# Kernel optimization log

Hardware: AMD Instinct MI355X
Metric: run time of the kernel (lower is better)

The kernel has to match this reference:

```python
import jax, jax.numpy as jnp
import numpy as np

NUM_HEADS = 16
NEG = -10000000.0


def setup_inputs() -> dict:
    key = jax.random.key(0)
    k1, k2, k3 = jax.random.split(key, 3)
    B, N, C = 4, 2048, 1024
    inputs = jax.random.normal(k1, (B, N, C), dtype=jnp.float32)
    # learned params (xavier-ish scale)
    W_qkv = jax.random.normal(k2, (C, 3 * C), dtype=jnp.float32) * 0.02
    W_proj = jax.random.normal(k3, (C, C), dtype=jnp.float32) * 0.02
    b_proj = jnp.zeros((C,), dtype=jnp.float32)
    attn_mask = jnp.ones((N, N), dtype=jnp.int32)      # >0 means keep
    padding_mask = jnp.zeros((B, N), dtype=jnp.int32)  # >0 means mask out
    return {"inputs": inputs, "attn_mask": attn_mask, "padding_mask": padding_mask,
            "W_qkv": W_qkv, "W_proj": W_proj, "b_proj": b_proj}


def reference(inputs, attn_mask, padding_mask, W_qkv, W_proj, b_proj):
    B, N, C = inputs.shape
    H = NUM_HEADS
    d = C // H
    scale = d ** -0.5
    qkv = inputs @ W_qkv                                   # [B,N,3C]
    qkv = qkv.reshape(B, N, 3, H, d).transpose(2, 0, 3, 1, 4)  # [3,B,H,N,d]
    q, k, v = qkv[0], qkv[1], qkv[2]
    scores = jnp.einsum('bhqd,bhkd->bhqk', q, k) * scale   # [B,H,N,N]
    scores = jnp.where(attn_mask > 0, scores, NEG)
    pm = padding_mask[:, None, None, :]                    # [B,1,1,N]
    scores = jnp.where(pm > 0, NEG, scores)
    attn = jax.nn.softmax(scores, axis=-1)
    x = jnp.einsum('bhqk,bhkd->bhqd', attn, v)             # [B,H,N,d]
    x = x.swapaxes(1, 2).reshape(B, N, C)
    return x @ W_proj + b_proj
```

## Files before the change

kernel.cpp:

```cpp
#include <hip/hip_runtime.h>

#define NEG -10000000.0f
#define QSCALE 0.18033688011112042f

typedef __attribute__((ext_vector_type(8))) short bf16x8;
typedef __attribute__((ext_vector_type(4))) float f32x4;

static __device__ __forceinline__ short f2bf(float f) {
    unsigned int u = __float_as_uint(f);
    unsigned int r = (u + 0x7fffu + ((u >> 16) & 1u)) >> 16;
    return (short)r;
}

static __device__ __forceinline__ unsigned pack_bf16_2(float a, float b) {
    unsigned ua = __float_as_uint(a) + 0x8000u;
    unsigned ub = __float_as_uint(b) + 0x8000u;
    return __builtin_amdgcn_perm(ub, ua, 0x07060302u);
}

static __device__ __forceinline__ void async_cp16(const void* g, void* l) {
    __builtin_amdgcn_global_load_lds(
        (const __attribute__((address_space(1))) unsigned int*)g,
        (__attribute__((address_space(3))) unsigned int*)l, 16, 0, 0);
}

__global__ void cvt_bf16(const float* __restrict__ src, short* __restrict__ dst, int n4) {
    int i = blockIdx.x * blockDim.x + threadIdx.x;
    if (i < n4) {
        float4 v = reinterpret_cast<const float4*>(src)[i];
        short4 o;
        o.x = f2bf(v.x); o.y = f2bf(v.y); o.z = f2bf(v.z); o.w = f2bf(v.w);
        reinterpret_cast<short4*>(dst)[i] = o;
    }
}

__global__ void transpose_cvt(const float* __restrict__ src, short* __restrict__ dst,
                              int rows, int cols) {
    __shared__ float tile[32][33];
    int bx = blockIdx.x * 32;
    int by = blockIdx.y * 32;
    int tx = threadIdx.x & 31, ty = threadIdx.x >> 5;
    for (int j = 0; j < 4; ++j)
        tile[ty + j * 8][tx] = src[(size_t)(by + ty + j * 8) * cols + bx + tx];
    __syncthreads();
    for (int j = 0; j < 4; ++j)
        dst[(size_t)(bx + ty + j * 8) * rows + by + tx] = f2bf(tile[tx][ty + j * 8]);
}

__global__ void mask_flags(const int* __restrict__ attn_mask,
                           const int* __restrict__ padding, int* __restrict__ flags) {
    int blk = blockIdx.x;
    int tid = threadIdx.x;
    if (blk == 512) {
        if (tid < 128) {
            int b = tid >> 5, kt = tid & 31;
            int any = 0;
            for (int j = 0; j < 64; ++j) any |= (padding[b * 2048 + kt * 64 + j] > 0);
            flags[512 + tid] = any;
        }
        return;
    }
    int qt = blk >> 5, kt = blk & 31;
    __shared__ int blockok;
    if (tid == 0) blockok = 1;
    __syncthreads();
    int ok = 1;
    for (int j = 0; j < 32; ++j) {
        int idx = j * 256 + tid;
        int qr = qt * 128 + (idx >> 6);
        int kc = kt * 64 + (idx & 63);
        ok &= (attn_mask[(size_t)qr * 2048 + kc] != 0);
    }
    if (!ok) blockok = 0;
    __syncthreads();
    if (tid == 0) flags[blk] = blockok;
}

#define G256_STAGE(BUF, MAT, HALF, C, KT, SRC, BASE)                              \
    {                                                                             \
        int rr_ = (HALF) * 128 + (C) * 64 + w * 8 + l8;                           \
        async_cp16(&SRC[(size_t)((BASE) + rr_) * 1024 + (KT) * 64 +               \
                        ((j8 ^ (rr_ & 7)) << 3)],                                 \
                   &smem[BUF][MAT][(HALF) * 128 + (C) * 64 + w * 8][0]);          \
    }

__global__ __launch_bounds__(512, 2) void gemm256_qkv(
    const short* __restrict__ A, const short* __restrict__ Bt,
    short* __restrict__ q_ws, short* __restrict__ k_ws, short* __restrict__ v_ws) {
    __shared__ __align__(16) short smem[2][2][256][64];

    int tid = threadIdx.x, lane = tid & 63, w = tid >> 6;
    int wm = w & 1, wn = w >> 1;
    int col = lane & 15, quad = lane >> 4;
    int l8 = lane >> 3, j8 = lane & 7;

    int nwg = gridDim.x * gridDim.y;
    int hw = blockIdx.y * gridDim.x + blockIdx.x;
    int logical = (hw & 7) * (nwg >> 3) + (hw >> 3);
    int bx = logical % gridDim.x, by = logical / gridDim.x;
    int m0 = by * 256, n0 = bx * 256;

    f32x4 acc[8][4] = {};

    G256_STAGE(0, 0, 0, 0, 0, A, m0) G256_STAGE(0, 0, 0, 1, 0, A, m0)
    G256_STAGE(0, 1, 0, 0, 0, Bt, n0) G256_STAGE(0, 1, 0, 1, 0, Bt, n0)
    G256_STAGE(0, 1, 1, 0, 0, Bt, n0) G256_STAGE(0, 1, 1, 1, 0, Bt, n0)
    G256_STAGE(0, 0, 1, 0, 0, A, m0) G256_STAGE(0, 0, 1, 1, 0, A, m0)

    for (int t = 0; t < 16; ++t) {
        int bt = t & 1, nb_ = bt ^ 1, ktn = t + 1;

        if (t < 15) {
            G256_STAGE(nb_, 0, 0, 0, ktn, A, m0) G256_STAGE(nb_, 0, 0, 1, ktn, A, m0)
            G256_STAGE(nb_, 1, 0, 0, ktn, Bt, n0) G256_STAGE(nb_, 1, 0, 1, ktn, Bt, n0)
            asm volatile("s_waitcnt vmcnt(4)" ::: "memory");
        } else {
            asm volatile("s_waitcnt vmcnt(0)" ::: "memory");
        }
        __builtin_amdgcn_s_barrier();
        __builtin_amdgcn_sched_barrier(0);

        bf16x8 bfr[4][2], af[4][2];
        for (int nt = 0; nt < 4; ++nt)
            for (int ks = 0; ks < 2; ++ks)
                bfr[nt][ks] = *reinterpret_cast<const bf16x8*>(
                    &smem[bt][1][wn * 64 + nt * 16 + col][((ks * 4 + quad) ^ (col & 7)) << 3]);
        for (int mt = 0; mt < 4; ++mt)
            for (int ks = 0; ks < 2; ++ks)
                af[mt][ks] = *reinterpret_cast<const bf16x8*>(
                    &smem[bt][0][wm * 128 + mt * 16 + col][((ks * 4 + quad) ^ (col & 7)) << 3]);
        __builtin_amdgcn_s_setprio(1);
        for (int ks = 0; ks < 2; ++ks)
            for (int mt = 0; mt < 4; ++mt)
                for (int nt = 0; nt < 4; ++nt)
                    acc[mt][nt] = __builtin_amdgcn_mfma_f32_16x16x32_bf16(af[mt][ks], bfr[nt][ks], acc[mt][nt], 0, 0, 0);
        __builtin_amdgcn_s_setprio(0);

        if (t < 15) {
            G256_STAGE(nb_, 1, 1, 0, ktn, Bt, n0) G256_STAGE(nb_, 1, 1, 1, ktn, Bt, n0)
            G256_STAGE(nb_, 0, 1, 0, ktn, A, m0) G256_STAGE(nb_, 0, 1, 1, ktn, A, m0)
        }
        for (int mt = 0; mt < 4; ++mt)
            for (int ks = 0; ks < 2; ++ks)
                af[mt][ks] = *reinterpret_cast<const bf16x8*>(
                    &smem[bt][0][wm * 128 + (4 + mt) * 16 + col][((ks * 4 + quad) ^ (col & 7)) << 3]);
        __builtin_amdgcn_s_setprio(1);
        for (int ks = 0; ks < 2; ++ks)
            for (int mt = 0; mt < 4; ++mt)
                for (int nt = 0; nt < 4; ++nt)
                    acc[4 + mt][nt] = __builtin_amdgcn_mfma_f32_16x16x32_bf16(af[mt][ks], bfr[nt][ks], acc[4 + mt][nt], 0, 0, 0);
        __builtin_amdgcn_s_setprio(0);
        __builtin_amdgcn_sched_barrier(0);
        __builtin_amdgcn_s_barrier();
    }

    short* L = &smem[0][0][0][0];
    int which = n0 >> 10;
    int cb = n0 & 1023;
    int b = m0 >> 11, nb = m0 & 2047, hb = cb >> 6;

    if (which == 2) {
        for (int mt = 0; mt < 8; ++mt)
            for (int nt = 0; nt < 4; ++nt) {
                int ml = wm * 128 + mt * 16 + quad * 4;
                int cl = wn * 64 + nt * 16 + col;
                int mp = (ml + 8 * cl) & 255;
                short4 pk;
                for (int r = 0; r < 4; ++r) ((short*)&pk)[r] = f2bf(acc[mt][nt][r]);
                *reinterpret_cast<short4*>(&L[cl * 256 + mp]) = pk;
            }
        __syncthreads();
        for (int it = 0; it < 16; ++it) {
            int chunk = it * 512 + tid;
            int c = chunk >> 5, j = chunk & 31;
            int h = hb + (c >> 6), dd = c & 63;
            int4 val = *reinterpret_cast<const int4*>(&L[c * 256 + (((j + c) & 31) << 3)]);
            *reinterpret_cast<int4*>(
                &v_ws[((size_t)((b * 16 + h) * 64 + dd)) * 2048 + nb + j * 8]) = val;
        }
    } else {
        short* dst = (which == 0) ? q_ws : k_ws;
        float scl = (which == 0) ? QSCALE : 1.0f;
        for (int mt = 0; mt < 8; ++mt)
            for (int nt = 0; nt < 4; ++nt)
                for (int r = 0; r < 4; ++r) {
                    int ml = wm * 128 + mt * 16 + quad * 4 + r;
                    int cl = wn * 64 + nt * 16 + col;
                    L[ml * 256 + ((cl + 8 * ml) & 255)] = f2bf(acc[mt][nt][r] * scl);
                }
        __syncthreads();
        for (int it = 0; it < 16; ++it) {
            int chunk = it * 512 + tid;
            int row = chunk >> 5, j = chunk & 31;
            int h = hb + (j >> 3), dd = (j & 7) * 8;
            int4 val = *reinterpret_cast<const int4*>(&L[row * 256 + (((j + row) & 31) << 3)]);
            *reinterpret_cast<int4*>(
                &dst[((size_t)(b * 16 + h) * 2048 + nb + row) * 64 + dd]) = val;
        }
    }
}

__global__ __launch_bounds__(256, 2) void gemm_bf16(
    const short* __restrict__ A, const short* __restrict__ Bt, int mode,
    short* __restrict__ q_ws, short* __restrict__ k_ws, short* __restrict__ v_ws,
    float* __restrict__ out, const float* __restrict__ bias) {
    const int K = 1024;
    __shared__ __align__(16) short smem[2][128][64];
    short (*As)[64] = smem[0];
    short (*Bs)[64] = smem[1];
    int tid = threadIdx.x, lane = tid & 63, w = tid >> 6;
    int wm = w & 1, wn = w >> 1;

    int nwg = gridDim.x * gridDim.y;
    int hw = blockIdx.y * gridDim.x + blockIdx.x;
    int logical = (hw & 7) * (nwg >> 3) + (hw >> 3);
    int bx = logical % gridDim.x, by = logical / gridDim.x;
    int m0 = by * 128, n0 = bx * 128;

    int col = lane & 15, quad = lane >> 4;
    int l8 = lane >> 3, j8 = lane & 7;

    f32x4 acc[4][4] = {};

    for (int k0 = 0; k0 < K; k0 += 64) {
        for (int c = 0; c < 4; ++c) {
            int rr = w * 32 + c * 8 + l8;
            int sw = (j8 ^ (rr & 7)) << 3;
            async_cp16(&A[(size_t)(m0 + rr) * K + k0 + sw], &As[w * 32 + c * 8][0]);
            async_cp16(&Bt[(size_t)(n0 + rr) * K + k0 + sw], &Bs[w * 32 + c * 8][0]);
        }
        __syncthreads();
        for (int ks = 0; ks < 2; ++ks) {
            bf16x8 af[4], bfr[4];
            for (int mt = 0; mt < 4; ++mt)
                af[mt] = *reinterpret_cast<const bf16x8*>(
                    &As[wm * 64 + mt * 16 + col][((ks * 4 + quad) ^ (col & 7)) << 3]);
            for (int nt = 0; nt < 4; ++nt)
                bfr[nt] = *reinterpret_cast<const bf16x8*>(
                    &Bs[wn * 64 + nt * 16 + col][((ks * 4 + quad) ^ (col & 7)) << 3]);
            for (int mt = 0; mt < 4; ++mt)
                for (int nt = 0; nt < 4; ++nt)
                    acc[mt][nt] = __builtin_amdgcn_mfma_f32_16x16x32_bf16(af[mt], bfr[nt], acc[mt][nt], 0, 0, 0);
        }
        __syncthreads();
    }

    short* L = &smem[0][0][0];

    if (mode == 0) {
        int which = n0 >> 10;
        int cb = n0 & 1023;
        int b = m0 >> 11, nb = m0 & 2047, hb = cb >> 6;
        if (which == 2) {
            for (int mt = 0; mt < 4; ++mt)
                for (int nt = 0; nt < 4; ++nt) {
                    int ml = wm * 64 + mt * 16 + quad * 4;
                    int cl = wn * 64 + nt * 16 + col;
                    int mp = (ml + 8 * cl) & 127;
                    short4 pk;
                    for (int r = 0; r < 4; ++r) ((short*)&pk)[r] = f2bf(acc[mt][nt][r]);
                    *reinterpret_cast<short4*>(&L[cl * 128 + mp]) = pk;
                }
            __syncthreads();
            for (int it = 0; it < 8; ++it) {
                int chunk = it * 256 + tid;
                int c = chunk >> 4, j = chunk & 15;
                int h = hb + (c >> 6), dd = c & 63;
                int4 val = *reinterpret_cast<const int4*>(&L[c * 128 + (((j + c) & 15) << 3)]);
                *reinterpret_cast<int4*>(
                    &v_ws[((size_t)((b * 16 + h) * 64 + dd)) * 2048 + nb + j * 8]) = val;
            }
        } else {
            short* dst = (which == 0) ? q_ws : k_ws;
            float scl = (which == 0) ? QSCALE : 1.0f;
            for (int mt = 0; mt < 4; ++mt)
                for (int nt = 0; nt < 4; ++nt)
                    for (int r = 0; r < 4; ++r) {
                        int ml = wm * 64 + mt * 16 + quad * 4 + r;
                        int cl = wn * 64 + nt * 16 + col;
                        L[ml * 128 + ((cl + 8 * ml) & 127)] = f2bf(acc[mt][nt][r] * scl);
                    }
            __syncthreads();
            for (int it = 0; it < 8; ++it) {
                int chunk = it * 256 + tid;
                int row = chunk >> 4, j = chunk & 15;
                int h = hb + (j >> 3), dd = (j & 7) * 8;
                int4 val = *reinterpret_cast<const int4*>(&L[row * 128 + (((j + row) & 15) << 3)]);
                *reinterpret_cast<int4*>(
                    &dst[((size_t)(b * 16 + h) * 2048 + nb + row) * 64 + dd]) = val;
            }
        }
    } else {
        float* Lf = reinterpret_cast<float*>(L);
        for (int half = 0; half < 2; ++half) {
            if (wm == half) {
                for (int mt = 0; mt < 4; ++mt)
                    for (int nt = 0; nt < 4; ++nt)
                        for (int r = 0; r < 4; ++r) {
                            int ml = mt * 16 + quad * 4 + r;
                            int cl = wn * 64 + nt * 16 + col;
                            Lf[ml * 128 + cl] = acc[mt][nt][r];
                        }
            }
            __syncthreads();
            for (int it = 0; it < 8; ++it) {
                int chunk = it * 256 + tid;
                int row = chunk >> 5, j = chunk & 31;
                float4 val = *reinterpret_cast<const float4*>(&Lf[row * 128 + j * 4]);
                float4 bv = *reinterpret_cast<const float4*>(&bias[n0 + j * 4]);
                val.x += bv.x; val.y += bv.y; val.z += bv.z; val.w += bv.w;
                *reinterpret_cast<float4*>(
                    &out[(size_t)(m0 + half * 64 + row) * 1024 + n0 + j * 4]) = val;
            }
            __syncthreads();
        }
    }
}

__global__ __launch_bounds__(256, 4) void flash_attn(
    const short* __restrict__ q_ws, const short* __restrict__ k_ws,
    const short* __restrict__ v_ws, const int* __restrict__ aflags,
    const int* __restrict__ pflags, const int* __restrict__ padding,
    const int* __restrict__ attn_mask, short* __restrict__ xb) {
    const int Nn = 2048, D = 64;
    __shared__ short QP[128][64];
    __shared__ short Ks[64][64];
    __shared__ short Vt[64][64];
    __shared__ __align__(16) float padb[64];

    int tid = threadIdx.x, lane = tid & 63, w = tid >> 6;
    int col = lane & 15, quad = lane >> 4;

    int hw = blockIdx.y * 16 + blockIdx.x;
    int logical = (hw & 7) * 128 + (hw >> 3);
    int bh = logical >> 4, qt = logical & 15;
    int b = bh >> 4, h = bh & 15;
    int q0 = qt * 128;

    int l8 = lane >> 3, j8 = lane & 7;

    for (int c = 0; c < 4; ++c) {
        int rr = w * 32 + c * 8 + l8;
        async_cp16(&q_ws[((size_t)bh * Nn + q0 + rr) * D + ((j8 ^ (rr & 7)) << 3)],
                   &QP[w * 32 + c * 8][0]);
    }
    __syncthreads();

    bf16x8 qf[2][2];
    for (int t = 0; t < 2; ++t)
        for (int ks = 0; ks < 2; ++ks)
            qf[t][ks] = *reinterpret_cast<const bf16x8*>(
                &QP[w * 32 + t * 16 + col][((ks * 4 + quad) ^ (col & 7)) << 3]);

    f32x4 oacc[2][4] = {};
    f32x4 lacc[2] = {};

    for (int kt = 0; kt < 32; ++kt) {
        int k0 = kt * 64;
        for (int c = 0; c < 2; ++c) {
            int rr = w * 16 + c * 8 + l8;
            int sw = (j8 ^ (rr & 7)) << 3;
            async_cp16(&k_ws[((size_t)bh * Nn + k0 + rr) * D + sw], &Ks[w * 16 + c * 8][0]);
            async_cp16(&v_ws[((size_t)bh * D + rr) * Nn + k0 + sw], &Vt[w * 16 + c * 8][0]);
        }
        int pflag = pflags[b * 32 + kt];
        if (pflag && tid < 64) padb[tid] = (padding[b * Nn + k0 + tid] > 0) ? NEG : 0.f;
        __syncthreads();

        f32x4 sacc[4][2] = {};
        for (int ks = 0; ks < 2; ++ks) {
            bf16x8 kf[4];
            for (int mt = 0; mt < 4; ++mt)
                kf[mt] = *reinterpret_cast<const bf16x8*>(
                    &Ks[mt * 16 + col][((ks * 4 + quad) ^ (col & 7)) << 3]);
            for (int mt = 0; mt < 4; ++mt)
                for (int t = 0; t < 2; ++t)
                    sacc[mt][t] = __builtin_amdgcn_mfma_f32_16x16x32_bf16(kf[mt], qf[t][ks], sacc[mt][t], 0, 0, 0);
        }

        if (!aflags[qt * 32 + kt]) {
            for (int mt = 0; mt < 4; ++mt)
                for (int t = 0; t < 2; ++t)
                    for (int r = 0; r < 4; ++r) {
                        int kc = k0 + mt * 16 + quad * 4 + r;
                        int qr = q0 + w * 32 + t * 16 + col;
                        if (attn_mask[(size_t)qr * Nn + kc] == 0) sacc[mt][t][r] = NEG;
                    }
        }
        if (pflag) {
            for (int mt = 0; mt < 4; ++mt) {
                f32x4 pb = *reinterpret_cast<const f32x4*>(&padb[mt * 16 + quad * 4]);
                for (int t = 0; t < 2; ++t)
                    for (int r = 0; r < 4; ++r) sacc[mt][t][r] += pb[r];
            }
        }

        for (int t = 0; t < 2; ++t) {
            int qrow = w * 32 + t * 16 + col;
            for (int mt = 0; mt < 4; ++mt) {
                f32x4 e;
                e[0] = __builtin_amdgcn_exp2f(sacc[mt][t][0]);
                e[1] = __builtin_amdgcn_exp2f(sacc[mt][t][1]);
                e[2] = __builtin_amdgcn_exp2f(sacc[mt][t][2]);
                e[3] = __builtin_amdgcn_exp2f(sacc[mt][t][3]);
                lacc[t] += e;
                unsigned p0 = pack_bf16_2(e[0], e[1]);
                unsigned p1 = pack_bf16_2(e[2], e[3]);
                int chunk = (mt * 2 + (quad >> 1)) ^ (col & 7);
                *reinterpret_cast<uint2*>(&QP[qrow][(chunk << 3) + ((quad & 1) << 2)]) =
                    make_uint2(p0, p1);
            }
        }

        for (int ks = 0; ks < 2; ++ks) {
            bf16x8 pf[2], vf[4];
            for (int t = 0; t < 2; ++t)
                pf[t] = *reinterpret_cast<const bf16x8*>(
                    &QP[w * 32 + t * 16 + col][((ks * 4 + quad) ^ (col & 7)) << 3]);
            for (int nt = 0; nt < 4; ++nt)
                vf[nt] = *reinterpret_cast<const bf16x8*>(
                    &Vt[nt * 16 + col][((ks * 4 + quad) ^ (col & 7)) << 3]);
            for (int t = 0; t < 2; ++t)
                for (int nt = 0; nt < 4; ++nt)
                    oacc[t][nt] = __builtin_amdgcn_mfma_f32_16x16x32_bf16(pf[t], vf[nt], oacc[t][nt], 0, 0, 0);
        }
        __syncthreads();
    }

    for (int t = 0; t < 2; ++t) {
        float ls = lacc[t][0] + lacc[t][1] + lacc[t][2] + lacc[t][3];
        ls += __shfl_xor(ls, 16);
        ls += __shfl_xor(ls, 32);
        for (int r = 0; r < 4; ++r) {
            float lv = __shfl(ls, quad * 4 + r, 16);
            float inv = 1.f / lv;
            int n = q0 + w * 32 + t * 16 + quad * 4 + r;
            for (int nt = 0; nt < 4; ++nt) {
                int dd = nt * 16 + col;
                xb[((size_t)(b * Nn + n)) * 1024 + h * 64 + dd] = f2bf(oacc[t][nt][r] * inv);
            }
        }
    }
}

extern "C" void kernel_launch(void* const* d_in, const int* in_sizes, int n_in,
                              void* d_out, int out_size, void* d_ws, size_t ws_size,
                              hipStream_t stream) {
    const float* x        = (const float*)d_in[0];
    const int* attn_mask  = (const int*)d_in[1];
    const int* padding    = (const int*)d_in[2];
    const float* W_qkv    = (const float*)d_in[3];
    const float* W_proj   = (const float*)d_in[4];
    const float* b_proj   = (const float*)d_in[5];
    float* out            = (float*)d_out;

    char* ws = (char*)d_ws;
    short* Xb   = (short*)(ws);
    short* Wqt  = (short*)(ws + (16u << 20));
    short* Wpt  = (short*)(ws + (22u << 20));
    short* q_ws = (short*)(ws + (24u << 20));
    short* k_ws = (short*)(ws + (40u << 20));
    short* v_ws = (short*)(ws + (56u << 20));
    short* xbuf = (short*)(ws + (72u << 20));
    int*  flags = (int*)(ws + (88u << 20));

    cvt_bf16<<<8192, 256, 0, stream>>>(x, Xb, 8388608 / 4);
    transpose_cvt<<<dim3(3072 / 32, 1024 / 32), 256, 0, stream>>>(W_qkv, Wqt, 1024, 3072);
    transpose_cvt<<<dim3(1024 / 32, 1024 / 32), 256, 0, stream>>>(W_proj, Wpt, 1024, 1024);
    mask_flags<<<513, 256, 0, stream>>>(attn_mask, padding, flags);

    gemm256_qkv<<<dim3(3072 / 256, 8192 / 256), 512, 0, stream>>>(
        Xb, Wqt, q_ws, k_ws, v_ws);

    flash_attn<<<dim3(16, 64), 256, 0, stream>>>(
        q_ws, k_ws, v_ws, flags, flags + 512, padding, attn_mask, xbuf);

    gemm_bf16<<<dim3(1024 / 128, 8192 / 128), 256, 0, stream>>>(
        xbuf, Wpt, 1, nullptr, nullptr, nullptr, out, b_proj);
}
```

Baseline: 284.8 us.

## Rewrite projection GEMM as 256x128 double-buffered pipelined kernel, merge weight transposes

Replaces the generic 128x128 bf16 GEMM used for the output projection with a dedicated 512-thread 256x128-tile kernel. The new kernel double-buffers shared memory, prefetches the next K-slice asynchronously in two halves interleaved with MFMA work, uses explicit vmcnt waits and raw barriers, and raises wave priority around the MFMA blocks. It also fuses the two weight transpose-convert launches into one kernel. The intent is to hide global load latency, cut barrier stalls and reduce launch overhead, at the cost of more LDS per block (128KB), which may limit occupancy.

```diff
diff --git a/kernel.cpp b/kernel.cpp
--- a/kernel.cpp
+++ b/kernel.cpp
@@ -34,17 +34,20 @@
     }
 }
 
-__global__ void transpose_cvt(const float* __restrict__ src, short* __restrict__ dst,
-                              int rows, int cols) {
+__global__ void transpose_cvt2(const float* __restrict__ s1, short* __restrict__ d1,
+                               const float* __restrict__ s2, short* __restrict__ d2) {
     __shared__ float tile[32][33];
-    int bx = blockIdx.x * 32;
+    const float* src; short* dst; int cols, bxx;
+    if (blockIdx.x < 96) { src = s1; dst = d1; cols = 3072; bxx = blockIdx.x; }
+    else                 { src = s2; dst = d2; cols = 1024; bxx = blockIdx.x - 96; }
+    int bx = bxx * 32;
     int by = blockIdx.y * 32;
     int tx = threadIdx.x & 31, ty = threadIdx.x >> 5;
     for (int j = 0; j < 4; ++j)
         tile[ty + j * 8][tx] = src[(size_t)(by + ty + j * 8) * cols + bx + tx];
     __syncthreads();
     for (int j = 0; j < 4; ++j)
-        dst[(size_t)(bx + ty + j * 8) * rows + by + tx] = f2bf(tile[tx][ty + j * 8]);
+        dst[(size_t)(bx + ty + j * 8) * 1024 + by + tx] = f2bf(tile[tx][ty + j * 8]);
 }
 
 __global__ void mask_flags(const int* __restrict__ attn_mask,
@@ -200,120 +203,101 @@
     }
 }
 
-__global__ __launch_bounds__(256, 2) void gemm_bf16(
-    const short* __restrict__ A, const short* __restrict__ Bt, int mode,
-    short* __restrict__ q_ws, short* __restrict__ k_ws, short* __restrict__ v_ws,
+#define PJ_STAGE_A(BUF, C, KT)                                                    \
+    {                                                                             \
+        int rr_ = (C) * 64 + w * 8 + l8;                                          \
+        async_cp16(&A[(size_t)(m0 + rr_) * 1024 + (KT) * 64 + ((j8 ^ l8) << 3)],  \
+                   smem + (BUF) * 16384 + ((C) * 64 + w * 8) * 64);               \
+    }
+#define PJ_STAGE_B(BUF, C, KT)                                                    \
+    {                                                                             \
+        int rr_ = (C) * 64 + w * 8 + l8;                                          \
+        async_cp16(&Bt[(size_t)(n0 + rr_) * 1024 + (KT) * 64 + ((j8 ^ l8) << 3)], \
+                   smem + 32768 + (BUF) * 8192 + ((C) * 64 + w * 8) * 64);        \
+    }
+
+__global__ __launch_bounds__(512, 2) void gemm256_proj(
+    const short* __restrict__ A, const short* __restrict__ Bt,
     float* __restrict__ out, const float* __restrict__ bias) {
-    const int K = 1024;
-    __shared__ __align__(16) short smem[2][128][64];
-    short (*As)[64] = smem[0];
-    short (*Bs)[64] = smem[1];
+    __shared__ __align__(16) short smem[65536];
+
     int tid = threadIdx.x, lane = tid & 63, w = tid >> 6;
-    int wm = w & 1, wn = w >> 1;
+    int wm = w & 3, wn = w >> 2;
+    int col = lane & 15, quad = lane >> 4;
+    int l8 = lane >> 3, j8 = lane & 7;
 
     int nwg = gridDim.x * gridDim.y;
     int hw = blockIdx.y * gridDim.x + blockIdx.x;
     int logical = (hw & 7) * (nwg >> 3) + (hw >> 3);
     int bx = logical % gridDim.x, by = logical / gridDim.x;
-    int m0 = by * 128, n0 = bx * 128;
-
-    int col = lane & 15, quad = lane >> 4;
-    int l8 = lane >> 3, j8 = lane & 7;
+    int m0 = by * 256, n0 = bx * 128;
 
     f32x4 acc[4][4] = {};
 
-    for (int k0 = 0; k0 < K; k0 += 64) {
-        for (int c = 0; c < 4; ++c) {
-            int rr = w * 32 + c * 8 + l8;
-            int sw = (j8 ^ (rr & 7)) << 3;
-            async_cp16(&A[(size_t)(m0 + rr) * K + k0 + sw], &As[w * 32 + c * 8][0]);
-            async_cp16(&Bt[(size_t)(n0 + rr) * K + k0 + sw], &Bs[w * 32 + c * 8][0]);
-        }
-        __syncthreads();
-        for (int ks = 0; ks < 2; ++ks) {
-            bf16x8 af[4], bfr[4];
-            for (int mt = 0; mt < 4; ++mt)
-                af[mt] = *reinterpret_cast<const bf16x8*>(
-                    &As[wm * 64 + mt * 16 + col][((ks * 4 + quad) ^ (col & 7)) << 3]);
+    PJ_STAGE_A(0, 0, 0) PJ_STAGE_A(0, 1, 0) PJ_STAGE_B(0, 0, 0)
+    PJ_STAGE_A(0, 2, 0) PJ_STAGE_A(0, 3, 0) PJ_STAGE_B(0, 1, 0)
+
+    for (int t = 0; t < 16; ++t) {
+        int bt = t & 1, nb_ = bt ^ 1, ktn = t + 1;
+        const short* Ab = smem + bt * 16384;
+        const short* Bb = smem + 32768 + bt * 8192;
+
+        if (t < 15) {
+            PJ_STAGE_A(nb_, 0, ktn) PJ_STAGE_A(nb_, 1, ktn) PJ_STAGE_B(nb_, 0, ktn)
+            asm volatile("s_waitcnt vmcnt(3)" ::: "memory");
+        } else {
+            asm volatile("s_waitcnt vmcnt(0)" ::: "memory");
+        }
+        __builtin_amdgcn_s_barrier();
+        __builtin_amdgcn_sched_barrier(0);
+
+        bf16x8 af[4], bfr[4];
+        for (int mt = 0; mt < 4; ++mt)
+            af[mt] = *reinterpret_cast<const bf16x8*>(
+                &Ab[(wm * 64 + mt * 16 + col) * 64 + ((quad ^ (col & 7)) << 3)]);
+        for (int nt = 0; nt < 4; ++nt)
+            bfr[nt] = *reinterpret_cast<const bf16x8*>(
+                &Bb[(wn * 64 + nt * 16 + col) * 64 + ((quad ^ (col & 7)) << 3)]);
+        __builtin_amdgcn_s_setprio(1);
+        for (int mt = 0; mt < 4; ++mt)
             for (int nt = 0; nt < 4; ++nt)
-                bfr[nt] = *reinterpret_cast<const bf16x8*>(
-                    &Bs[wn * 64 + nt * 16 + col][((ks * 4 + quad) ^ (col & 7)) << 3]);
-            for (int mt = 0; mt < 4; ++mt)
-                for (int nt = 0; nt < 4; ++nt)
-                    acc[mt][nt] = __builtin_amdgcn_mfma_f32_16x16x32_bf16(af[mt], bfr[nt], acc[mt][nt], 0, 0, 0);
-        }
-        __syncthreads();
-    }
-
-    short* L = &smem[0][0][0];
-
-    if (mode == 0) {
-        int which = n0 >> 10;
-        int cb = n0 & 1023;
-        int b = m0 >> 11, nb = m0 & 2047, hb = cb >> 6;
-        if (which == 2) {
-            for (int mt = 0; mt < 4; ++mt)
-                for (int nt = 0; nt < 4; ++nt) {
-                    int ml = wm * 64 + mt * 16 + quad * 4;
-                    int cl = wn * 64 + nt * 16 + col;
-                    int mp = (ml + 8 * cl) & 127;
-                    short4 pk;
-                    for (int r = 0; r < 4; ++r) ((short*)&pk)[r] = f2bf(acc[mt][nt][r]);
-                    *reinterpret_cast<short4*>(&L[cl * 128 + mp]) = pk;
-                }
-            __syncthreads();
-            for (int it = 0; it < 8; ++it) {
-                int chunk = it * 256 + tid;
-                int c = chunk >> 4, j = chunk & 15;
-                int h = hb + (c >> 6), dd = c & 63;
-                int4 val = *reinterpret_cast<const int4*>(&L[c * 128 + (((j + c) & 15) << 3)]);
-                *reinterpret_cast<int4*>(
-                    &v_ws[((size_t)((b * 16 + h) * 64 + dd)) * 2048 + nb + j * 8]) = val;
+                acc[mt][nt] = __builtin_amdgcn_mfma_f32_16x16x32_bf16(af[mt], bfr[nt], acc[mt][nt], 0, 0, 0);
+        __builtin_amdgcn_s_setprio(0);
+
+        if (t < 15) {
+            PJ_STAGE_A(nb_, 2, ktn) PJ_STAGE_A(nb_, 3, ktn) PJ_STAGE_B(nb_, 1, ktn)
+        }
+        for (int mt = 0; mt < 4; ++mt)
+            af[mt] = *reinterpret_cast<const bf16x8*>(
+                &Ab[(wm * 64 + mt * 16 + col) * 64 + (((4 + quad) ^ (col & 7)) << 3)]);
+        for (int nt = 0; nt < 4; ++nt)
+            bfr[nt] = *reinterpret_cast<const bf16x8*>(
+                &Bb[(wn * 64 + nt * 16 + col) * 64 + (((4 + quad) ^ (col & 7)) << 3)]);
+        __builtin_amdgcn_s_setprio(1);
+        for (int mt = 0; mt < 4; ++mt)
+            for (int nt = 0; nt < 4; ++nt)
+                acc[mt][nt] = __builtin_amdgcn_mfma_f32_16x16x32_bf16(af[mt], bfr[nt], acc[mt][nt], 0, 0, 0);
+        __builtin_amdgcn_s_setprio(0);
+        __builtin_amdgcn_sched_barrier(0);
+        __builtin_amdgcn_s_barrier();
+    }
+
+    float* Lf = reinterpret_cast<float*>(smem);
+    for (int mt = 0; mt < 4; ++mt)
+        for (int nt = 0; nt < 4; ++nt)
+            for (int r = 0; r < 4; ++r) {
+                int ml = wm * 64 + mt * 16 + quad * 4 + r;
+                int cl = wn * 64 + nt * 16 + col;
+                Lf[ml * 128 + cl] = acc[mt][nt][r];
             }
-        } else {
-            short* dst = (which == 0) ? q_ws : k_ws;
-            float scl = (which == 0) ? QSCALE : 1.0f;
-            for (int mt = 0; mt < 4; ++mt)
-                for (int nt = 0; nt < 4; ++nt)
-                    for (int r = 0; r < 4; ++r) {
-                        int ml = wm * 64 + mt * 16 + quad * 4 + r;
-                        int cl = wn * 64 + nt * 16 + col;
-                        L[ml * 128 + ((cl + 8 * ml) & 127)] = f2bf(acc[mt][nt][r] * scl);
-                    }
-            __syncthreads();
-            for (int it = 0; it < 8; ++it) {
-                int chunk = it * 256 + tid;
-                int row = chunk >> 4, j = chunk & 15;
-                int h = hb + (j >> 3), dd = (j & 7) * 8;
-                int4 val = *reinterpret_cast<const int4*>(&L[row * 128 + (((j + row) & 15) << 3)]);
-                *reinterpret_cast<int4*>(
-                    &dst[((size_t)(b * 16 + h) * 2048 + nb + row) * 64 + dd]) = val;
-            }
-        }
-    } else {
-        float* Lf = reinterpret_cast<float*>(L);
-        for (int half = 0; half < 2; ++half) {
-            if (wm == half) {
-                for (int mt = 0; mt < 4; ++mt)
-                    for (int nt = 0; nt < 4; ++nt)
-                        for (int r = 0; r < 4; ++r) {
-                            int ml = mt * 16 + quad * 4 + r;
-                            int cl = wn * 64 + nt * 16 + col;
-                            Lf[ml * 128 + cl] = acc[mt][nt][r];
-                        }
-            }
-            __syncthreads();
-            for (int it = 0; it < 8; ++it) {
-                int chunk = it * 256 + tid;
-                int row = chunk >> 5, j = chunk & 31;
-                float4 val = *reinterpret_cast<const float4*>(&Lf[row * 128 + j * 4]);
-                float4 bv = *reinterpret_cast<const float4*>(&bias[n0 + j * 4]);
-                val.x += bv.x; val.y += bv.y; val.z += bv.z; val.w += bv.w;
-                *reinterpret_cast<float4*>(
-                    &out[(size_t)(m0 + half * 64 + row) * 1024 + n0 + j * 4]) = val;
-            }
-            __syncthreads();
-        }
+    __syncthreads();
+    for (int it = 0; it < 16; ++it) {
+        int chunk = it * 512 + tid;
+        int row = chunk >> 5, j = chunk & 31;
+        float4 val = *reinterpret_cast<const float4*>(&Lf[row * 128 + j * 4]);
+        float4 bv = *reinterpret_cast<const float4*>(&bias[n0 + j * 4]);
+        val.x += bv.x; val.y += bv.y; val.z += bv.z; val.w += bv.w;
+        *reinterpret_cast<float4*>(&out[(size_t)(m0 + row) * 1024 + n0 + j * 4]) = val;
     }
 }
 
@@ -465,8 +449,7 @@
     int*  flags = (int*)(ws + (88u << 20));
 
     cvt_bf16<<<8192, 256, 0, stream>>>(x, Xb, 8388608 / 4);
-    transpose_cvt<<<dim3(3072 / 32, 1024 / 32), 256, 0, stream>>>(W_qkv, Wqt, 1024, 3072);
-    transpose_cvt<<<dim3(1024 / 32, 1024 / 32), 256, 0, stream>>>(W_proj, Wpt, 1024, 1024);
+    transpose_cvt2<<<dim3(128, 32), 256, 0, stream>>>(W_qkv, Wqt, W_proj, Wpt);
     mask_flags<<<513, 256, 0, stream>>>(attn_mask, padding, flags);
 
     gemm256_qkv<<<dim3(3072 / 256, 8192 / 256), 512, 0, stream>>>(
@@ -475,6 +458,6 @@
     flash_attn<<<dim3(16, 64), 256, 0, stream>>>(
         q_ws, k_ws, v_ws, flags, flags + 512, padding, attn_mask, xbuf);
 
-    gemm_bf16<<<dim3(1024 / 128, 8192 / 128), 256, 0, stream>>>(
-        xbuf, Wpt, 1, nullptr, nullptr, nullptr, out, b_proj);
-}
+    gemm256_proj<<<dim3(1024 / 128, 8192 / 256), 512, 0, stream>>>(
+        xbuf, Wpt, out, b_proj);
+}
```

Result: slower. 291.4 us (+2.3%).
